# Optimization experiments

Measured on AMD Instinct MI355X. Metric: run time of the kernel, lower is better.

Reference implementation:

```python
import jax, jax.numpy as jnp
import numpy as np
from jax import lax

K = 3          # kernel size
PAD = 1        # (K-1)//2
C = 64         # channels
RED = 16       # channel-attention reduction


def conv2d(x, w, b=None):
    # x [B,C,H,W], w [O,I,kh,kw]
    out = lax.conv_general_dilated(x, w, (1, 1), 'SAME',
                                   dimension_numbers=('NCHW', 'OIHW', 'NCHW'))
    if b is not None:
        out = out + b[None, :, None, None]
    return out


def rcab(x, w1, b1, w2, b2, caw1, cab1, caw2, cab2):
    res = conv2d(x, w1, b1)
    res = jax.nn.relu(res)
    res = conv2d(res, w2, b2)
    # channel attention: global avg pool -> 1x1 conv -> relu -> 1x1 conv -> sigmoid
    y = jnp.mean(res, axis=(2, 3), keepdims=True)
    y = jax.nn.relu(conv2d(y, caw1, cab1))
    y = jax.nn.sigmoid(conv2d(y, caw2, cab2))
    return res * y + x


def deform_conv(x, inter, fea, off_w, off_b, mask_w, mask_b, weight):
    # Modulated deformable conv: offsets/mask predicted from concat(inter, fea).
    B, Cc, H, W = x.shape
    KK = K * K
    guide = jnp.concatenate([inter, fea], axis=1)
    offset = conv2d(guide, off_w, off_b)                    # [B, 2*KK, H, W]
    mask = 2.0 * jax.nn.sigmoid(conv2d(guide, mask_w, mask_b))  # [B, KK, H, W]
    off = offset.reshape(B, KK, 2, H, W)
    oy, ox = off[:, :, 0], off[:, :, 1]                     # [B, KK, H, W]

    ky = (jnp.arange(KK) // K - PAD).astype(x.dtype)        # kernel tap y offsets
    kx = (jnp.arange(KK) % K - PAD).astype(x.dtype)
    ii = jnp.arange(H, dtype=x.dtype)[None, None, :, None]
    jj = jnp.arange(W, dtype=x.dtype)[None, None, None, :]
    ys = ii + ky[None, :, None, None] + oy                  # [B, KK, H, W]
    xs = jj + kx[None, :, None, None] + ox

    y0 = jnp.floor(ys); x0 = jnp.floor(xs)
    wy1 = ys - y0; wy0 = 1.0 - wy1
    wx1 = xs - x0; wx0 = 1.0 - wx1
    y0i = y0.astype(jnp.int32); x0i = x0.astype(jnp.int32)
    y1i = y0i + 1; x1i = x0i + 1

    x_flat = x.reshape(B, Cc, H * W)

    def gather(yi, xi):
        valid = ((yi >= 0) & (yi < H) & (xi >= 0) & (xi < W)).astype(x.dtype)
        idx = jnp.clip(yi, 0, H - 1) * W + jnp.clip(xi, 0, W - 1)   # [B,KK,H,W]
        idx = idx.reshape(B, KK * H * W)
        g = jax.vmap(lambda f, i: jnp.take(f, i, axis=1))(x_flat, idx)
        return g.reshape(B, Cc, KK, H, W) * valid[:, None]

    val = (gather(y0i, x0i) * (wy0 * wx0)[:, None]
           + gather(y0i, x1i) * (wy0 * wx1)[:, None]
           + gather(y1i, x0i) * (wy1 * wx0)[:, None]
           + gather(y1i, x1i) * (wy1 * wx1)[:, None])     # [B,C,KK,H,W]
    val = val * mask[:, None]
    w_flat = weight.reshape(weight.shape[0], Cc, KK)        # [O,I,KK]
    return jnp.einsum('bckhw,ock->bohw', val, w_flat)


def setup_inputs() -> dict:
    key = jax.random.key(0)
    ks = jax.random.split(key, 20)
    B, H, W = 4, 192, 192
    f32 = jnp.float32
    d = {
        'x':     jax.random.normal(ks[0], (B, C, H, W), f32),
        'inter': jax.random.normal(ks[1], (B, C, H, W), f32),
        'fea':   jax.random.normal(ks[2], (B, C, H, W), f32),
        # RCAB
        'rcab_w1': jax.random.normal(ks[3], (C, C, 3, 3), f32) * 0.05,
        'rcab_b1': jnp.zeros((C,), f32),
        'rcab_w2': jax.random.normal(ks[4], (C, C, 3, 3), f32) * 0.05,
        'rcab_b2': jnp.zeros((C,), f32),
        'ca_w1': jax.random.normal(ks[5], (C // RED, C, 1, 1), f32) * 0.05,
        'ca_b1': jnp.zeros((C // RED,), f32),
        'ca_w2': jax.random.normal(ks[6], (C, C // RED, 1, 1), f32) * 0.05,
        'ca_b2': jnp.zeros((C,), f32),
        # deformable conv offset/mask branch (input = concat(inter, fea) -> 2C)
        'off_w': jax.random.normal(ks[7], (2 * K * K, 2 * C, 3, 3), f32) * 0.01,
        'off_b': jnp.zeros((2 * K * K,), f32),
        'mask_w': jax.random.normal(ks[8], (K * K, 2 * C, 3, 3), f32) * 0.01,
        'mask_b': jnp.zeros((K * K,), f32),
        'deform_w': jax.random.normal(ks[9], (C, C, K, K), f32) * 0.05,
        # final conv
        'conv_w': jax.random.normal(ks[10], (C, C, 3, 3), f32) * 0.05,
        'conv_b': jnp.zeros((C,), f32),
    }
    return d


def reference(x, inter, fea, rcab_w1, rcab_b1, rcab_w2, rcab_b2,
              ca_w1, ca_b1, ca_w2, ca_b2,
              off_w, off_b, mask_w, mask_b, deform_w, conv_w, conv_b):
    out1 = rcab(x, rcab_w1, rcab_b1, rcab_w2, rcab_b2, ca_w1, ca_b1, ca_w2, ca_b2)
    out2 = deform_conv(out1, inter, fea, off_w, off_b, mask_w, mask_b, deform_w)
    return conv2d(out2 + out1, conv_w, conv_b)
```

## Files before the change

kernel.cpp:

```cpp
#include <hip/hip_runtime.h>
#include <hip/hip_bf16.h>
#include <hip/hip_fp16.h>
#include <math.h>

#define HSZ 192
#define WSZ 192
#define HWSZ (192*192)
#define PH 194
#define PP (PH*PH)
#define NB 4

typedef __attribute__((ext_vector_type(8))) short short8;
typedef __attribute__((ext_vector_type(4))) float f32x4;

__device__ inline unsigned short f2bf(float f) { __hip_bfloat16 h = __float2bfloat16(f); return *(unsigned short*)&h; }
__device__ inline float bf2f(__hip_bfloat16 h) { return __bfloat162float(h); }
__device__ inline float bflo(unsigned u) { return __uint_as_float(u << 16); }
__device__ inline float bfhi(unsigned u) { return __uint_as_float(u & 0xffff0000u); }

#define GLDS(SRC, DST) __builtin_amdgcn_global_load_lds( \
    (const __attribute__((address_space(1))) unsigned int*)(const void*)(SRC), \
    (__attribute__((address_space(3))) unsigned int*)(void*)(DST), 16, 0, 0)

#define MFMA(A,B,C) __builtin_amdgcn_mfma_f32_16x16x32_bf16((A),(B),(C),0,0,0)

__global__ void zb2_k(__hip_bfloat16* xn, __hip_bfloat16* r1, __hip_bfloat16* out1,
                      __hip_bfloat16* cat) {
  int job = blockIdx.y;
  __hip_bfloat16* buf = job == 0 ? xn : job == 1 ? r1 : job == 2 ? out1 : cat;
  int Cn = (job == 3) ? 128 : 64;
  int cg8 = Cn >> 3;
  int tot = NB * 772 * cg8;
  int idx = blockIdx.x * 256 + threadIdx.x;
  if (idx >= tot) return;
  int cg = idx % cg8; int rem = idx / cg8;
  int e = rem % 772; int b = rem / 772;
  int h, w2;
  if (e < 194) { h = 0; w2 = e; }
  else if (e < 388) { h = 193; w2 = e - 194; }
  else if (e < 580) { h = e - 388 + 1; w2 = 0; }
  else { h = e - 580 + 1; w2 = 193; }
  uint4 z = make_uint4(0, 0, 0, 0);
  *(uint4*)&buf[(((size_t)b * PH + h) * PH + w2) * Cn + cg * 8] = z;
}

__global__ void wts_k(const float* __restrict__ rw1, const float* __restrict__ rw2,
                      const float* __restrict__ cw, const float* __restrict__ offw,
                      const float* __restrict__ maskw, const float* __restrict__ offb,
                      const float* __restrict__ maskb, const float* __restrict__ dwv,
                      short* wt1, short* wt2c, short* wtf, short* wtom, float* ob,
                      short* wtb, float* meanz) {
  int job = blockIdx.y;
  int idx = blockIdx.x * 256 + threadIdx.x;
  if (job < 3) {
    const float* src = job == 0 ? rw1 : job == 1 ? rw2 : cw;
    short* dst = job == 0 ? wt1 : job == 1 ? wt2c : wtf;
    int kk = idx >> 12, rem = idx & 4095;
    int co = rem >> 6, ci = rem & 63;
    dst[idx] = (short)f2bf(src[(co * 64 + ci) * 9 + kk]);
  } else if (job == 3) {
    int kk = idx >> 12, rem = idx & 4095;
    int co = rem >> 7, ci = rem & 127;
    float v = 0.f;
    if (co < 18) v = offw[(co * 128 + ci) * 9 + kk];
    else if (co < 27) v = maskw[((co - 18) * 128 + ci) * 9 + kk];
    wtom[idx] = (short)f2bf(v);
    if (idx < 32) ob[idx] = idx < 18 ? offb[idx] : (idx < 27 ? maskb[idx - 18] : 0.f);
  } else {
    int o = idx / 576, rem = idx - o * 576;
    int kk = rem >> 6, ci = rem & 63;
    wtb[idx] = (short)f2bf(dwv[(o * 64 + ci) * 9 + kk]);
    if (blockIdx.x == 0 && threadIdx.x < 256) meanz[threadIdx.x] = 0.f;
  }
}

__global__ __launch_bounds__(256) void cvt_k(const float* __restrict__ x,
    const float* __restrict__ inter, const float* __restrict__ fea,
    __hip_bfloat16* __restrict__ xn, __hip_bfloat16* __restrict__ cat) {
  int job = blockIdx.z;
  const float* src = job == 0 ? x : job == 1 ? inter : fea;
  __hip_bfloat16* dst = job == 0 ? xn : cat;
  int Cdst = job == 0 ? 64 : 128;
  int coff = job == 2 ? 64 : 0;
  __shared__ float s[64][65];
  int p0 = blockIdx.x * 64; int b = blockIdx.y;
  int lane = threadIdx.x & 63, g = threadIdx.x >> 6;
#pragma unroll
  for (int i = 0; i < 16; ++i) {
    int c = i * 4 + g;
    s[c][lane] = src[((size_t)b * 64 + c) * HWSZ + p0 + lane];
  }
  __syncthreads();
  int pix = threadIdx.x >> 2, cg = threadIdx.x & 3;
  int h = p0 / WSZ, w0 = p0 - h * WSZ + pix;
  size_t addr = (((size_t)b * PH + h + 1) * PH + 1 + w0) * Cdst + coff + cg * 16;
  unsigned pk2[8];
#pragma unroll
  for (int t = 0; t < 8; ++t)
    pk2[t] = (unsigned)f2bf(s[cg * 16 + 2 * t][pix]) | ((unsigned)f2bf(s[cg * 16 + 2 * t + 1][pix]) << 16);
  *(uint4*)&dst[addr]     = make_uint4(pk2[0], pk2[1], pk2[2], pk2[3]);
  *(uint4*)&dst[addr + 8] = make_uint4(pk2[4], pk2[5], pk2[6], pk2[7]);
}

template<int OUT_MODE, bool RELU, bool MEANACC>
__global__ __launch_bounds__(256, 3) void conv_mfma_k(
    const __hip_bfloat16* __restrict__ inp, const short* __restrict__ wt,
    const float* __restrict__ bias, __hip_bfloat16* __restrict__ outB,
    float* __restrict__ outF, float* __restrict__ meanout) {
  int flat = (blockIdx.x & 7) * 96 + (blockIdx.x >> 3);
  const int b = flat / 192, h = flat - (flat / 192) * 192;
  const int tid = threadIdx.x, lane = tid & 63, wid = tid >> 6;
  const int q = lane >> 4, r16 = lane & 15;
  __shared__ __align__(16) short tile[2][200 * 64];
  __shared__ float smean[4][64];

  const __hip_bfloat16* base = inp + ((size_t)b * PH + h) * (PH * 64);
#define STAGE(BUF, R) do { \
    const char* gb_ = (const char*)(base + (size_t)(R) * (PH * 64)); \
    for (int s_ = wid; s_ < 25; s_ += 4) { \
      int pix_ = 8 * s_ + (lane >> 3); \
      const char* src_ = gb_ + pix_ * 128 + ((((lane & 7) ^ ((lane >> 3) & 7))) << 4); \
      GLDS(src_, tile[BUF] + s_ * 512); \
    } \
  } while (0)

  STAGE(0, 0);

  f32x4 acc[3][4];
  if (OUT_MODE == 0) {
#pragma unroll
    for (int nf = 0; nf < 4; ++nf) {
      float4 bv = *(const float4*)&bias[nf * 16 + q * 4];
      f32x4 v; v[0] = bv.x; v[1] = bv.y; v[2] = bv.z; v[3] = bv.w;
      acc[0][nf] = v; acc[1][nf] = v; acc[2][nf] = v;
    }
  } else {
#pragma unroll
    for (int nf = 0; nf < 4; ++nf) {
      float bs = bias[nf * 16 + r16];
      f32x4 v; v[0] = bs; v[1] = bs; v[2] = bs; v[3] = bs;
      acc[0][nf] = v; acc[1][nf] = v; acc[2][nf] = v;
    }
  }

  short8 bfr[2][2][4];
  {
    const short* wk0 = wt + r16 * 64 + q * 8;
#pragma unroll
    for (int nf = 0; nf < 4; ++nf) {
      bfr[0][0][nf] = *(const short8*)(wk0 + nf * 1024);
      bfr[0][1][nf] = *(const short8*)(wk0 + nf * 1024 + 32);
    }
  }
  __syncthreads();

  const int wm0 = wid * 48;
#pragma unroll
  for (int ky = 0; ky < 3; ++ky) {
    const int cb = ky & 1;
    if (ky < 2) STAGE(cb ^ 1, ky + 1);
#pragma unroll
    for (int kx = 0; kx < 3; ++kx) {
      const int kk = ky * 3 + kx;
      const int cur = kk & 1;
      if (kk < 8) {
        const short* wk = wt + (kk + 1) * 4096 + r16 * 64 + q * 8;
#pragma unroll
        for (int nf = 0; nf < 4; ++nf) {
          bfr[cur ^ 1][0][nf] = *(const short8*)(wk + nf * 1024);
          bfr[cur ^ 1][1][nf] = *(const short8*)(wk + nf * 1024 + 32);
        }
      }
#pragma unroll
      for (int mf = 0; mf < 3; ++mf) {
        int pix = wm0 + mf * 16 + r16 + kx;
        const char* ab = (const char*)tile[cb] + pix * 128;
        int sw = (pix & 7) << 4;
        short8 a0 = *(const short8*)(ab + ((q << 4) ^ sw));
        short8 a1 = *(const short8*)(ab + (((q + 4) << 4) ^ sw));
#pragma unroll
        for (int nf = 0; nf < 4; ++nf) {
          if (OUT_MODE == 0) {
            acc[mf][nf] = MFMA(bfr[cur][0][nf], a0, acc[mf][nf]);
            acc[mf][nf] = MFMA(bfr[cur][1][nf], a1, acc[mf][nf]);
          } else {
            acc[mf][nf] = MFMA(a0, bfr[cur][0][nf], acc[mf][nf]);
            acc[mf][nf] = MFMA(a1, bfr[cur][1][nf], acc[mf][nf]);
          }
        }
      }
    }
    __syncthreads();
  }
#undef STAGE

  if (MEANACC) {
    float t[4][4];
#pragma unroll
    for (int nf = 0; nf < 4; ++nf)
#pragma unroll
      for (int rg = 0; rg < 4; ++rg)
        t[nf][rg] = acc[0][nf][rg] + acc[1][nf][rg] + acc[2][nf][rg];
#pragma unroll
    for (int m = 1; m < 16; m <<= 1)
#pragma unroll
      for (int nf = 0; nf < 4; ++nf)
#pragma unroll
        for (int rg = 0; rg < 4; ++rg)
          t[nf][rg] += __shfl_xor(t[nf][rg], m);
    if (r16 == 0)
#pragma unroll
      for (int nf = 0; nf < 4; ++nf)
#pragma unroll
        for (int rg = 0; rg < 4; ++rg)
          smean[wid][nf * 16 + q * 4 + rg] = t[nf][rg];
    __syncthreads();
    if (tid < 64)
      atomicAdd(&meanout[b * 64 + tid],
                (smean[0][tid] + smean[1][tid] + smean[2][tid] + smean[3][tid]) * (1.f / 36864.f));
  }

  if (OUT_MODE == 0) {
#pragma unroll
    for (int mf = 0; mf < 3; ++mf)
#pragma unroll
      for (int nf = 0; nf < 4; ++nf) {
        f32x4 v = acc[mf][nf];
        if (RELU) { v[0] = fmaxf(v[0], 0.f); v[1] = fmaxf(v[1], 0.f); v[2] = fmaxf(v[2], 0.f); v[3] = fmaxf(v[3], 0.f); }
        unsigned lo = (unsigned)f2bf(v[0]) | ((unsigned)f2bf(v[1]) << 16);
        unsigned hi = (unsigned)f2bf(v[2]) | ((unsigned)f2bf(v[3]) << 16);
        int pix = wm0 + mf * 16 + r16;
        int byteoff = (pix * 128 + nf * 32 + q * 8) ^ ((pix & 7) << 4);
        *(uint2*)((char*)tile[1] + byteoff) = make_uint2(lo, hi);
      }
    __syncthreads();
    char* orow = (char*)outB + ((((size_t)b * PH + h + 1) * PH + 1) * 64) * 2;
    for (int s = wid; s < 24; s += 4) {
      int pix = 8 * s + (lane >> 3);
      int g16 = ((lane & 7) ^ (pix & 7)) << 4;
      uint4 d = *(const uint4*)((const char*)tile[1] + pix * 128 + g16);
      *(uint4*)(orow + pix * 128 + ((lane & 7) << 4)) = d;
    }
  } else {
    float* ob2 = outF + (size_t)b * 64 * HWSZ + h * WSZ;
#pragma unroll
    for (int mf = 0; mf < 3; ++mf)
#pragma unroll
      for (int nf = 0; nf < 4; ++nf) {
        int pix0 = wm0 + mf * 16 + q * 4;
        int co = nf * 16 + r16;
        *(f32x4*)&ob2[(size_t)co * HWSZ + pix0] = acc[mf][nf];
      }
  }
}

__global__ __launch_bounds__(256, 3) void offmask_mfma_k(
    const __hip_bfloat16* __restrict__ cat, const short* __restrict__ wt2,
    const float* __restrict__ ob, float* __restrict__ om) {
  const int h = blockIdx.x, b = blockIdx.y;
  const int tid = threadIdx.x, lane = tid & 63, wid = tid >> 6;
  const int q = lane >> 4, r16 = lane & 15;
  __shared__ __align__(16) short tile[200 * 128];

  f32x4 acc[3][2];
#pragma unroll
  for (int nf = 0; nf < 2; ++nf) {
    float bs = ob[nf * 16 + r16];
    f32x4 v; v[0] = bs; v[1] = bs; v[2] = bs; v[3] = bs;
    acc[0][nf] = v; acc[1][nf] = v; acc[2][nf] = v;
  }
  const char* gb = (const char*)(cat + ((size_t)b * PH + h) * (PH * 128));
  const int wm0 = wid * 48;

  short8 bfr[2][4][2];
  {
    const short* wk0 = wt2 + r16 * 128 + q * 8;
#pragma unroll
    for (int c4 = 0; c4 < 4; ++c4) {
      bfr[0][c4][0] = *(const short8*)(wk0 + c4 * 32);
      bfr[0][c4][1] = *(const short8*)(wk0 + 2048 + c4 * 32);
    }
  }

#pragma unroll
  for (int r = 0; r < 3; ++r) {
    __syncthreads();
    for (int s = wid; s < 50; s += 4) {
      int pix = 4 * s + (lane >> 4);
      const char* src = gb + (size_t)r * (PH * 256) + pix * 256
                      + ((((lane & 15) ^ (pix & 15))) << 4);
      GLDS(src, tile + s * 512);
    }
    __syncthreads();
#pragma unroll
    for (int kx = 0; kx < 3; ++kx) {
      const int kk = r * 3 + kx;
      const int cur = kk & 1;
      if (kk < 8) {
        const short* wk = wt2 + (kk + 1) * 4096 + r16 * 128 + q * 8;
#pragma unroll
        for (int c4 = 0; c4 < 4; ++c4) {
          bfr[cur ^ 1][c4][0] = *(const short8*)(wk + c4 * 32);
          bfr[cur ^ 1][c4][1] = *(const short8*)(wk + 2048 + c4 * 32);
        }
      }
#pragma unroll
      for (int mf = 0; mf < 3; ++mf) {
        int pix = wm0 + mf * 16 + r16 + kx;
        const char* ab = (const char*)tile + pix * 256;
        int sw = (pix & 15) << 4;
        short8 a0 = *(const short8*)(ab + ((q << 4) ^ sw));
        short8 a1 = *(const short8*)(ab + (((4 + q) << 4) ^ sw));
        short8 a2 = *(const short8*)(ab + (((8 + q) << 4) ^ sw));
        short8 a3 = *(const short8*)(ab + (((12 + q) << 4) ^ sw));
        acc[mf][0] = MFMA(a0, bfr[cur][0][0], acc[mf][0]); acc[mf][1] = MFMA(a0, bfr[cur][0][1], acc[mf][1]);
        acc[mf][0] = MFMA(a1, bfr[cur][1][0], acc[mf][0]); acc[mf][1] = MFMA(a1, bfr[cur][1][1], acc[mf][1]);
        acc[mf][0] = MFMA(a2, bfr[cur][2][0], acc[mf][0]); acc[mf][1] = MFMA(a2, bfr[cur][2][1], acc[mf][1]);
        acc[mf][0] = MFMA(a3, bfr[cur][3][0], acc[mf][0]); acc[mf][1] = MFMA(a3, bfr[cur][3][1], acc[mf][1]);
      }
    }
  }
#pragma unroll
  for (int mf = 0; mf < 3; ++mf)
#pragma unroll
    for (int nf = 0; nf < 2; ++nf) {
      int co = nf * 16 + r16;
      if (co < 27) {
        f32x4 v = acc[mf][nf];
        if (co >= 18) {
          v[0] = 2.f / (1.f + expf(-v[0])); v[1] = 2.f / (1.f + expf(-v[1]));
          v[2] = 2.f / (1.f + expf(-v[2])); v[3] = 2.f / (1.f + expf(-v[3]));
        }
        *(f32x4*)&om[((size_t)(b * 27 + co)) * HWSZ + h * WSZ + wm0 + mf * 16 + q * 4] = v;
      }
    }
}

__global__ __launch_bounds__(256) void out1_k(const __hip_bfloat16* __restrict__ res, const __hip_bfloat16* __restrict__ xn,
    const float* __restrict__ mean, const float* __restrict__ w1, const float* __restrict__ b1,
    const float* __restrict__ w2, const float* __restrict__ b2,
    __hip_bfloat16* __restrict__ out1) {
  int idx = blockIdx.x * 256 + threadIdx.x;
  int b = idx / 294912; int rem = idx - b * 294912;
  int p = rem >> 3, c8 = rem & 7;
  int lane = threadIdx.x & 63, wid = threadIdx.x >> 6;

  __shared__ float s_t[4];
  {
    float prod = w1[wid * 64 + lane] * mean[b * 64 + lane];
#pragma unroll
    for (int m = 1; m < 64; m <<= 1) prod += __shfl_xor(prod, m);
    if (lane == 0) s_t[wid] = fmaxf(prod + b1[wid], 0.f);
  }
  __syncthreads();
  float t0 = s_t[0], t1 = s_t[1], t2 = s_t[2], t3 = s_t[3];

  int hh = p / WSZ, ww = p - hh * WSZ;
  size_t off = ((size_t)b * PP + (size_t)(hh + 1) * PH + ww + 1) * 64 + c8 * 8;
  const __hip_bfloat16* rp = res + off;
  const __hip_bfloat16* xp = xn + off;
  __hip_bfloat16* op = out1 + off;
  unsigned pk[4];
#pragma unroll
  for (int t = 0; t < 4; ++t) {
    float y0, y1;
    {
      int c = c8 * 8 + 2 * t;
      const float4 wv0 = *(const float4*)&w2[c * 4];
      const float4 wv1 = *(const float4*)&w2[(c + 1) * 4];
      float v0 = b2[c]     + wv0.x * t0 + wv0.y * t1 + wv0.z * t2 + wv0.w * t3;
      float v1 = b2[c + 1] + wv1.x * t0 + wv1.y * t1 + wv1.z * t2 + wv1.w * t3;
      y0 = 1.f / (1.f + expf(-v0));
      y1 = 1.f / (1.f + expf(-v1));
    }
    float o0 = bf2f(rp[2 * t]) * y0 + bf2f(xp[2 * t]);
    float o1 = bf2f(rp[2 * t + 1]) * y1 + bf2f(xp[2 * t + 1]);
    pk[t] = (unsigned)f2bf(o0) | ((unsigned)f2bf(o1) << 16);
  }
  *(uint4*)op = make_uint4(pk[0], pk[1], pk[2], pk[3]);
}

__global__ __launch_bounds__(256) void deform_mfma_k(
    const __hip_bfloat16* __restrict__ nhwc, const float* __restrict__ om,
    const short* __restrict__ wtb, __hip_bfloat16* __restrict__ fin) {
  int blk = (blockIdx.x & 7) * 288 + (blockIdx.x >> 3);
  int b = blk / 576;
  int p0 = (blk - b * 576) * 64;
  int tid = threadIdx.x, lane = tid & 63, wid = tid >> 6;
  int q = lane >> 4, r16 = lane & 15;
  __shared__ __align__(16) short sA[2][64][64];
  __shared__ __half2 s_bw[2][9][64];
  __shared__ int s_pk[9][64];

  const float* omb = om + (size_t)b * 27 * HWSZ + p0;
  for (int e = tid; e < 576; e += 256) {
    int kk = e >> 6, pix = e & 63;
    int p = p0 + pix;
    int h = p / WSZ, w2 = p - h * WSZ;
    float oy = omb[(size_t)(2 * kk) * HWSZ + pix];
    float ox = omb[(size_t)(2 * kk + 1) * HWSZ + pix];
    float m2 = omb[(size_t)(18 + kk) * HWSZ + pix];
    float ys = (float)(h + kk / 3 - 1) + oy;
    float xs = (float)(w2 + kk % 3 - 1) + ox;
    float y0f = floorf(ys), x0f = floorf(xs);
    float wy1 = ys - y0f, wx1 = xs - x0f;
    float wy0 = 1.f - wy1, wx0 = 1.f - wx1;
    int y0 = (int)y0f, x0i = (int)x0f;
    int y1 = y0 + 1, x1 = x0i + 1;
    float vy0 = (y0 >= 0 && y0 < HSZ) ? 1.f : 0.f;
    float vx0 = (x0i >= 0 && x0i < WSZ) ? 1.f : 0.f;
    float vy1 = (y1 >= 0 && y1 < HSZ) ? 1.f : 0.f;
    float vx1 = (x1 >= 0 && x1 < WSZ) ? 1.f : 0.f;
    int y0c = min(max(y0, 0), HSZ - 1), x0c = min(max(x0i, 0), WSZ - 1);
    int y1c = min(max(y1, 0), HSZ - 1), x1c = min(max(x1, 0), WSZ - 1);
    s_bw[0][kk][pix] = __floats2half2_rn(wy0 * wx0 * m2 * vy0 * vx0, wy0 * wx1 * m2 * vy0 * vx1);
    s_bw[1][kk][pix] = __floats2half2_rn(wy1 * wx0 * m2 * vy1 * vx0, wy1 * wx1 * m2 * vy1 * vx1);
    s_pk[kk][pix] = ((((y0c + 1) * PH) + x0c + 1) << 2) | ((y1c - y0c) << 1) | (x1c - x0c);
  }
  __syncthreads();

  const __hip_bfloat16* nb = nhwc + (size_t)b * PP * 64;
  const int spix = tid >> 2, lg = tid & 3;
  const int rsw = (r16 & 7) << 4;

  uint4 Pa0, Pb0, Qa0, Qb0, Ra0, Rb0, Sa0, Sb0;
  uint4 Pa1, Pb1, Qa1, Qb1, Ra1, Rb1, Sa1, Sb1;
  float2 wab0, wcd0, wab1, wcd1;

#define ISSUE_R(KK, Pa,Pb,Qa,Qb,Ra,Rb,Sa,Sb, Wab, Wcd) do { \
    Wab = __half22float2(s_bw[0][KK][spix]); \
    Wcd = __half22float2(s_bw[1][KK][spix]); \
    int pk_ = s_pk[KK][spix]; \
    int i00_ = pk_ >> 2, dy_ = (pk_ >> 1) & 1, dx_ = pk_ & 1; \
    const __hip_bfloat16* g_ = nb + (size_t)i00_ * 64 + lg * 16; \
    Pa = *(const uint4*)g_;                     Pb = *(const uint4*)(g_ + 8); \
    Qa = *(const uint4*)(g_ + dx_ * 64);        Qb = *(const uint4*)(g_ + dx_ * 64 + 8); \
    Ra = *(const uint4*)(g_ + dy_ * (PH * 64)); Rb = *(const uint4*)(g_ + dy_ * (PH * 64) + 8); \
    Sa = *(const uint4*)(g_ + (dy_ * PH + dx_) * 64); Sb = *(const uint4*)(g_ + (dy_ * PH + dx_) * 64 + 8); \
  } while (0)
#define CMB(J, PA,QA,RA,SA, Wab, Wcd, OUT) do { \
    const unsigned* pa_ = (const unsigned*)&PA; const unsigned* qa_ = (const unsigned*)&QA; \
    const unsigned* ra_ = (const unsigned*)&RA; const unsigned* sa_ = (const unsigned*)&SA; \
    float lo_ = Wab.x * bflo(pa_[J]) + Wab.y * bflo(qa_[J]) + Wcd.x * bflo(ra_[J]) + Wcd.y * bflo(sa_[J]); \
    float hi_ = Wab.x * bfhi(pa_[J]) + Wab.y * bfhi(qa_[J]) + Wcd.x * bfhi(ra_[J]) + Wcd.y * bfhi(sa_[J]); \
    OUT = (unsigned)f2bf(lo_) | ((unsigned)f2bf(hi_) << 16); \
  } while (0)
#define CSTORE_R(BUFOFF, Pa,Pb,Qa,Qb,Ra,Rb,Sa,Sb, Wab, Wcd) do { \
    unsigned oa_[4], ob_[4]; \
    CMB(0, Pa,Qa,Ra,Sa, Wab, Wcd, oa_[0]); CMB(1, Pa,Qa,Ra,Sa, Wab, Wcd, oa_[1]); \
    CMB(2, Pa,Qa,Ra,Sa, Wab, Wcd, oa_[2]); CMB(3, Pa,Qa,Ra,Sa, Wab, Wcd, oa_[3]); \
    CMB(0, Pb,Qb,Rb,Sb, Wab, Wcd, ob_[0]); CMB(1, Pb,Qb,Rb,Sb, Wab, Wcd, ob_[1]); \
    CMB(2, Pb,Qb,Rb,Sb, Wab, Wcd, ob_[2]); CMB(3, Pb,Qb,Rb,Sb, Wab, Wcd, ob_[3]); \
    char* dst_ = (char*)sA + (BUFOFF) + spix * 128; \
    *(uint4*)(dst_ + ((((lg * 2) ^ (spix & 7))) << 4))     = make_uint4(oa_[0], oa_[1], oa_[2], oa_[3]); \
    *(uint4*)(dst_ + ((((lg * 2 + 1) ^ (spix & 7))) << 4)) = make_uint4(ob_[0], ob_[1], ob_[2], ob_[3]); \
  } while (0)

  ISSUE_R(0, Pa0,Pb0,Qa0,Qb0,Ra0,Rb0,Sa0,Sb0, wab0, wcd0);
  CSTORE_R(0, Pa0,Pb0,Qa0,Qb0,Ra0,Rb0,Sa0,Sb0, wab0, wcd0);
  ISSUE_R(1, Pa0,Pb0,Qa0,Qb0,Ra0,Rb0,Sa0,Sb0, wab0, wcd0);
  ISSUE_R(2, Pa1,Pb1,Qa1,Qb1,Ra1,Rb1,Sa1,Sb1, wab1, wcd1);

  f32x4 acc0 = (f32x4){0.f, 0.f, 0.f, 0.f};
  f32x4 acc1 = (f32x4){0.f, 0.f, 0.f, 0.f};
  f32x4 acc2 = (f32x4){0.f, 0.f, 0.f, 0.f};
  f32x4 acc3 = (f32x4){0.f, 0.f, 0.f, 0.f};
  const short* wrow = wtb + (size_t)(wid * 16 + r16) * 576;
  const char* a0base = (const char*)sA + r16 * 128;
  const char* a1base = (const char*)sA + (r16 + 16) * 128;
  const char* a2base = (const char*)sA + (r16 + 32) * 128;
  const char* a3base = (const char*)sA + (r16 + 48) * 128;

#pragma unroll
  for (int kk = 0; kk < 9; ++kk) {
    const int bo = (kk & 1) * 8192;
    __syncthreads();
#pragma unroll
    for (int s = 0; s < 2; ++s) {
      short8 wf = *(const short8*)(wrow + kk * 64 + s * 32 + q * 8);
      int off = bo + ((s * 64 + q * 16) ^ rsw);
      acc0 = MFMA(wf, *(const short8*)(a0base + off), acc0);
      acc1 = MFMA(wf, *(const short8*)(a1base + off), acc1);
      acc2 = MFMA(wf, *(const short8*)(a2base + off), acc2);
      acc3 = MFMA(wf, *(const short8*)(a3base + off), acc3);
    }
    if (kk < 8) {
      const int nbo = ((kk + 1) & 1) * 8192;
      if ((kk & 1) == 0) {
        CSTORE_R(nbo, Pa0,Pb0,Qa0,Qb0,Ra0,Rb0,Sa0,Sb0, wab0, wcd0);
        if (kk + 3 <= 8) ISSUE_R(kk + 3, Pa0,Pb0,Qa0,Qb0,Ra0,Rb0,Sa0,Sb0, wab0, wcd0);
      } else {
        CSTORE_R(nbo, Pa1,Pb1,Qa1,Qb1,Ra1,Rb1,Sa1,Sb1, wab1, wcd1);
        if (kk + 3 <= 8) ISSUE_R(kk + 3, Pa1,Pb1,Qa1,Qb1,Ra1,Rb1,Sa1,Sb1, wab1, wcd1);
      }
    }
  }

  int h0 = p0 / WSZ, w0 = p0 - h0 * WSZ;
  size_t ro = ((size_t)(h0 + 1) * PH + w0 + 1) * 64;
  const __hip_bfloat16* resid = nb + ro;
  __hip_bfloat16* fp = fin + (size_t)b * PP * 64 + ro;
#pragma unroll
  for (int nf = 0; nf < 4; ++nf) {
    f32x4 av = nf == 0 ? acc0 : nf == 1 ? acc1 : nf == 2 ? acc2 : acc3;
    int pix = r16 + nf * 16;
    int co = wid * 16 + q * 4;
    const unsigned* rr = (const unsigned*)(resid + (size_t)pix * 64 + co);
    unsigned r0 = rr[0], r1 = rr[1];
    float o0 = av[0] + bflo(r0);
    float o1 = av[1] + bfhi(r0);
    float o2 = av[2] + bflo(r1);
    float o3 = av[3] + bfhi(r1);
    uint2 pk2 = make_uint2((unsigned)f2bf(o0) | ((unsigned)f2bf(o1) << 16),
                           (unsigned)f2bf(o2) | ((unsigned)f2bf(o3) << 16));
    *(uint2*)(fp + (size_t)pix * 64 + co) = pk2;
  }
#undef ISSUE_R
#undef CMB
#undef CSTORE_R
}

extern "C" void kernel_launch(void* const* d_in, const int* in_sizes, int n_in,
                              void* d_out, int out_size, void* d_ws, size_t ws_size,
                              hipStream_t stream) {
  (void)in_sizes; (void)n_in; (void)out_size; (void)ws_size;
  const float* x     = (const float*)d_in[0];
  const float* inter = (const float*)d_in[1];
  const float* fea   = (const float*)d_in[2];
  const float* rw1   = (const float*)d_in[3];
  const float* rb1   = (const float*)d_in[4];
  const float* rw2   = (const float*)d_in[5];
  const float* rb2   = (const float*)d_in[6];
  const float* caw1  = (const float*)d_in[7];
  const float* cab1  = (const float*)d_in[8];
  const float* caw2  = (const float*)d_in[9];
  const float* cab2  = (const float*)d_in[10];
  const float* offw  = (const float*)d_in[11];
  const float* offb  = (const float*)d_in[12];
  const float* maskw = (const float*)d_in[13];
  const float* maskb = (const float*)d_in[14];
  const float* dw    = (const float*)d_in[15];
  const float* cw    = (const float*)d_in[16];
  const float* cb    = (const float*)d_in[17];

  char* w = (char*)d_ws;
  const size_t P64 = (size_t)NB * PP * 64 * 2 + 4096;
  const size_t PCAT = (size_t)NB * PP * 128 * 2 + 4096;
  __hip_bfloat16* xn   = (__hip_bfloat16*)(w);
  __hip_bfloat16* r1   = (__hip_bfloat16*)(w + P64);
  __hip_bfloat16* res  = (__hip_bfloat16*)(w + 2 * P64);
  __hip_bfloat16* out1 = (__hip_bfloat16*)(w + 3 * P64);
  __hip_bfloat16* cat  = (__hip_bfloat16*)(w + 4 * P64);
  char* tail = w + 4 * P64 + PCAT;
  short* wt1  = (short*)tail; tail += 73728;
  short* wt2c = (short*)tail; tail += 73728;
  short* wtf  = (short*)tail; tail += 73728;
  short* wtom = (short*)tail; tail += 73728;
  float* obb  = (float*)tail; tail += 128;
  short* wtb  = (short*)tail; tail += 73728;
  float* mean = (float*)tail; tail += 1024;
  float* omb  = (float*)res;
  __hip_bfloat16* fin = r1;

  zb2_k<<<dim3(194, 4), 256, 0, stream>>>(xn, r1, out1, cat);
  wts_k<<<dim3(144, 5), 256, 0, stream>>>(rw1, rw2, cw, offw, maskw, offb, maskb, dw,
                                          wt1, wt2c, wtf, wtom, obb, wtb, mean);
  cvt_k<<<dim3(576, 4, 3), 256, 0, stream>>>(x, inter, fea, xn, cat);

  conv_mfma_k<0, true , false><<<768, 256, 0, stream>>>(xn, wt1, rb1, r1, nullptr, nullptr);
  conv_mfma_k<0, false, true ><<<768, 256, 0, stream>>>(r1, wt2c, rb2, res, nullptr, mean);
  out1_k<<<4608, 256, 0, stream>>>(res, xn, mean, caw1, cab1, caw2, cab2, out1);
  offmask_mfma_k<<<dim3(192, 4), 256, 0, stream>>>(cat, wtom, obb, omb);
  deform_mfma_k<<<NB * 576, 256, 0, stream>>>(out1, omb, wtb, fin);
  conv_mfma_k<1, false, false><<<768, 256, 0, stream>>>(fin, wtf, cb, nullptr, (float*)d_out, nullptr);
}
```

Baseline: 255.6 us.

## Merge conv1 and offset/mask conv into one launch, widen deform blocks

```diff
diff --git a/kernel.cpp b/kernel.cpp
--- a/kernel.cpp
+++ b/kernel.cpp
@@ -24,10 +24,10 @@
 
 #define MFMA(A,B,C) __builtin_amdgcn_mfma_f32_16x16x32_bf16((A),(B),(C),0,0,0)
 
-__global__ void zb2_k(__hip_bfloat16* xn, __hip_bfloat16* r1, __hip_bfloat16* out1,
+__global__ void zb2_k(__hip_bfloat16* xn, __hip_bfloat16* r1, __hip_bfloat16* res,
                       __hip_bfloat16* cat) {
   int job = blockIdx.y;
-  __hip_bfloat16* buf = job == 0 ? xn : job == 1 ? r1 : job == 2 ? out1 : cat;
+  __hip_bfloat16* buf = job == 0 ? xn : job == 1 ? r1 : job == 2 ? res : cat;
   int Cn = (job == 3) ? 128 : 64;
   int cg8 = Cn >> 3;
   int tot = NB * 772 * cg8;
@@ -103,16 +103,14 @@
 }
 
 template<int OUT_MODE, bool RELU, bool MEANACC>
-__global__ __launch_bounds__(256, 3) void conv_mfma_k(
+__device__ __forceinline__ void conv_body(int vbid, short* tbuf, float* smean,
     const __hip_bfloat16* __restrict__ inp, const short* __restrict__ wt,
     const float* __restrict__ bias, __hip_bfloat16* __restrict__ outB,
     float* __restrict__ outF, float* __restrict__ meanout) {
-  int flat = (blockIdx.x & 7) * 96 + (blockIdx.x >> 3);
+  int flat = (vbid & 7) * 96 + (vbid >> 3);
   const int b = flat / 192, h = flat - (flat / 192) * 192;
   const int tid = threadIdx.x, lane = tid & 63, wid = tid >> 6;
   const int q = lane >> 4, r16 = lane & 15;
-  __shared__ __align__(16) short tile[2][200 * 64];
-  __shared__ float smean[4][64];
 
   const __hip_bfloat16* base = inp + ((size_t)b * PH + h) * (PH * 64);
 #define STAGE(BUF, R) do { \
@@ -120,7 +118,7 @@
     for (int s_ = wid; s_ < 25; s_ += 4) { \
       int pix_ = 8 * s_ + (lane >> 3); \
       const char* src_ = gb_ + pix_ * 128 + ((((lane & 7) ^ ((lane >> 3) & 7))) << 4); \
-      GLDS(src_, tile[BUF] + s_ * 512); \
+      GLDS(src_, tbuf + (BUF) * 12800 + s_ * 512); \
     } \
   } while (0)
 
@@ -174,7 +172,7 @@
 #pragma unroll
       for (int mf = 0; mf < 3; ++mf) {
         int pix = wm0 + mf * 16 + r16 + kx;
-        const char* ab = (const char*)tile[cb] + pix * 128;
+        const char* ab = (const char*)(tbuf + cb * 12800) + pix * 128;
         int sw = (pix & 7) << 4;
         short8 a0 = *(const short8*)(ab + ((q << 4) ^ sw));
         short8 a1 = *(const short8*)(ab + (((q + 4) << 4) ^ sw));
@@ -213,14 +211,15 @@
       for (int nf = 0; nf < 4; ++nf)
 #pragma unroll
         for (int rg = 0; rg < 4; ++rg)
-          smean[wid][nf * 16 + q * 4 + rg] = t[nf][rg];
+          smean[wid * 64 + nf * 16 + q * 4 + rg] = t[nf][rg];
     __syncthreads();
     if (tid < 64)
       atomicAdd(&meanout[b * 64 + tid],
-                (smean[0][tid] + smean[1][tid] + smean[2][tid] + smean[3][tid]) * (1.f / 36864.f));
+                (smean[tid] + smean[64 + tid] + smean[128 + tid] + smean[192 + tid]) * (1.f / 36864.f));
   }
 
   if (OUT_MODE == 0) {
+    short* t1 = tbuf + 12800;
 #pragma unroll
     for (int mf = 0; mf < 3; ++mf)
 #pragma unroll
@@ -231,14 +230,14 @@
         unsigned hi = (unsigned)f2bf(v[2]) | ((unsigned)f2bf(v[3]) << 16);
         int pix = wm0 + mf * 16 + r16;
         int byteoff = (pix * 128 + nf * 32 + q * 8) ^ ((pix & 7) << 4);
-        *(uint2*)((char*)tile[1] + byteoff) = make_uint2(lo, hi);
+        *(uint2*)((char*)t1 + byteoff) = make_uint2(lo, hi);
       }
     __syncthreads();
     char* orow = (char*)outB + ((((size_t)b * PH + h + 1) * PH + 1) * 64) * 2;
     for (int s = wid; s < 24; s += 4) {
       int pix = 8 * s + (lane >> 3);
       int g16 = ((lane & 7) ^ (pix & 7)) << 4;
-      uint4 d = *(const uint4*)((const char*)tile[1] + pix * 128 + g16);
+      uint4 d = *(const uint4*)((const char*)t1 + pix * 128 + g16);
       *(uint4*)(orow + pix * 128 + ((lane & 7) << 4)) = d;
     }
   } else {
@@ -254,13 +253,13 @@
   }
 }
 
-__global__ __launch_bounds__(256, 3) void offmask_mfma_k(
+__device__ __forceinline__ void offmask_body(int vbid, short* tbuf,
     const __hip_bfloat16* __restrict__ cat, const short* __restrict__ wt2,
     const float* __restrict__ ob, float* __restrict__ om) {
-  const int h = blockIdx.x, b = blockIdx.y;
+  int flat = (vbid & 7) * 96 + (vbid >> 3);
+  const int b = flat / 192, h = flat - (flat / 192) * 192;
   const int tid = threadIdx.x, lane = tid & 63, wid = tid >> 6;
   const int q = lane >> 4, r16 = lane & 15;
-  __shared__ __align__(16) short tile[200 * 128];
 
   f32x4 acc[3][2];
 #pragma unroll
@@ -289,7 +288,7 @@
       int pix = 4 * s + (lane >> 4);
       const char* src = gb + (size_t)r * (PH * 256) + pix * 256
                       + ((((lane & 15) ^ (pix & 15))) << 4);
-      GLDS(src, tile + s * 512);
+      GLDS(src, tbuf + s * 512);
     }
     __syncthreads();
 #pragma unroll
@@ -307,7 +306,7 @@
 #pragma unroll
       for (int mf = 0; mf < 3; ++mf) {
         int pix = wm0 + mf * 16 + r16 + kx;
-        const char* ab = (const char*)tile + pix * 256;
+        const char* ab = (const char*)tbuf + pix * 256;
         int sw = (pix & 15) << 4;
         short8 a0 = *(const short8*)(ab + ((q << 4) ^ sw));
         short8 a1 = *(const short8*)(ab + (((4 + q) << 4) ^ sw));
@@ -336,10 +335,33 @@
     }
 }
 
-__global__ __launch_bounds__(256) void out1_k(const __hip_bfloat16* __restrict__ res, const __hip_bfloat16* __restrict__ xn,
+template<int OUT_MODE, bool RELU, bool MEANACC>
+__global__ __launch_bounds__(256, 3) void conv_mfma_k(
+    const __hip_bfloat16* __restrict__ inp, const short* __restrict__ wt,
+    const float* __restrict__ bias, __hip_bfloat16* __restrict__ outB,
+    float* __restrict__ outF, float* __restrict__ meanout) {
+  __shared__ __align__(16) short tile[2 * 12800];
+  __shared__ float smean[256];
+  conv_body<OUT_MODE, RELU, MEANACC>(blockIdx.x, tile, smean, inp, wt, bias, outB, outF, meanout);
+}
+
+__global__ __launch_bounds__(256, 3) void c1om_k(
+    const __hip_bfloat16* __restrict__ xn, const short* __restrict__ wt1,
+    const float* __restrict__ rb1, __hip_bfloat16* __restrict__ r1,
+    const __hip_bfloat16* __restrict__ cat, const short* __restrict__ wtom,
+    const float* __restrict__ obb, float* __restrict__ omb) {
+  __shared__ __align__(16) short tile[2 * 12800];
+  int g = blockIdx.x >> 3;
+  int vid = ((g >> 1) << 3) | (blockIdx.x & 7);
+  if ((g & 1) == 0)
+    conv_body<0, true, false>(vid, tile, nullptr, xn, wt1, rb1, r1, nullptr, nullptr);
+  else
+    offmask_body(vid, tile, cat, wtom, obb, omb);
+}
+
+__global__ __launch_bounds__(256) void out1_k(__hip_bfloat16* __restrict__ res, const __hip_bfloat16* __restrict__ xn,
     const float* __restrict__ mean, const float* __restrict__ w1, const float* __restrict__ b1,
-    const float* __restrict__ w2, const float* __restrict__ b2,
-    __hip_bfloat16* __restrict__ out1) {
+    const float* __restrict__ w2, const float* __restrict__ b2) {
   int idx = blockIdx.x * 256 + threadIdx.x;
   int b = idx / 294912; int rem = idx - b * 294912;
   int p = rem >> 3, c8 = rem & 7;
@@ -357,9 +379,8 @@
 
   int hh = p / WSZ, ww = p - hh * WSZ;
   size_t off = ((size_t)b * PP + (size_t)(hh + 1) * PH + ww + 1) * 64 + c8 * 8;
-  const __hip_bfloat16* rp = res + off;
+  __hip_bfloat16* rp = res + off;
   const __hip_bfloat16* xp = xn + off;
-  __hip_bfloat16* op = out1 + off;
   unsigned pk[4];
 #pragma unroll
   for (int t = 0; t < 4; ++t) {
@@ -377,24 +398,24 @@
     float o1 = bf2f(rp[2 * t + 1]) * y1 + bf2f(xp[2 * t + 1]);
     pk[t] = (unsigned)f2bf(o0) | ((unsigned)f2bf(o1) << 16);
   }
-  *(uint4*)op = make_uint4(pk[0], pk[1], pk[2], pk[3]);
-}
-
-__global__ __launch_bounds__(256) void deform_mfma_k(
+  *(uint4*)rp = make_uint4(pk[0], pk[1], pk[2], pk[3]);
+}
+
+__global__ __launch_bounds__(512) void deform_mfma_k(
     const __hip_bfloat16* __restrict__ nhwc, const float* __restrict__ om,
     const short* __restrict__ wtb, __hip_bfloat16* __restrict__ fin) {
-  int blk = (blockIdx.x & 7) * 288 + (blockIdx.x >> 3);
-  int b = blk / 576;
-  int p0 = (blk - b * 576) * 64;
+  int blk = (blockIdx.x & 7) * 144 + (blockIdx.x >> 3);
+  int b = blk / 288;
+  int p0 = (blk - b * 288) * 128;
   int tid = threadIdx.x, lane = tid & 63, wid = tid >> 6;
   int q = lane >> 4, r16 = lane & 15;
-  __shared__ __align__(16) short sA[2][64][64];
-  __shared__ __half2 s_bw[2][9][64];
-  __shared__ int s_pk[9][64];
+  __shared__ __align__(16) short sA[2][128][64];
+  __shared__ __half2 s_bw[2][9][128];
+  __shared__ int s_pk[9][128];
 
   const float* omb = om + (size_t)b * 27 * HWSZ + p0;
-  for (int e = tid; e < 576; e += 256) {
-    int kk = e >> 6, pix = e & 63;
+  for (int e = tid; e < 1152; e += 512) {
+    int kk = e >> 7, pix = e & 127;
     int p = p0 + pix;
     int h = p / WSZ, w2 = p - h * WSZ;
     float oy = omb[(size_t)(2 * kk) * HWSZ + pix];
@@ -465,15 +486,16 @@
   f32x4 acc1 = (f32x4){0.f, 0.f, 0.f, 0.f};
   f32x4 acc2 = (f32x4){0.f, 0.f, 0.f, 0.f};
   f32x4 acc3 = (f32x4){0.f, 0.f, 0.f, 0.f};
-  const short* wrow = wtb + (size_t)(wid * 16 + r16) * 576;
-  const char* a0base = (const char*)sA + r16 * 128;
-  const char* a1base = (const char*)sA + (r16 + 16) * 128;
-  const char* a2base = (const char*)sA + (r16 + 32) * 128;
-  const char* a3base = (const char*)sA + (r16 + 48) * 128;
+  const int cs = wid & 3, ph = wid >> 2;
+  const short* wrow = wtb + (size_t)(cs * 16 + r16) * 576;
+  const char* a0base = (const char*)sA + (ph * 64 + r16) * 128;
+  const char* a1base = (const char*)sA + (ph * 64 + r16 + 16) * 128;
+  const char* a2base = (const char*)sA + (ph * 64 + r16 + 32) * 128;
+  const char* a3base = (const char*)sA + (ph * 64 + r16 + 48) * 128;
 
 #pragma unroll
   for (int kk = 0; kk < 9; ++kk) {
-    const int bo = (kk & 1) * 8192;
+    const int bo = (kk & 1) * 16384;
     __syncthreads();
 #pragma unroll
     for (int s = 0; s < 2; ++s) {
@@ -485,7 +507,7 @@
       acc3 = MFMA(wf, *(const short8*)(a3base + off), acc3);
     }
     if (kk < 8) {
-      const int nbo = ((kk + 1) & 1) * 8192;
+      const int nbo = ((kk + 1) & 1) * 16384;
       if ((kk & 1) == 0) {
         CSTORE_R(nbo, Pa0,Pb0,Qa0,Qb0,Ra0,Rb0,Sa0,Sb0, wab0, wcd0);
         if (kk + 3 <= 8) ISSUE_R(kk + 3, Pa0,Pb0,Qa0,Qb0,Ra0,Rb0,Sa0,Sb0, wab0, wcd0);
@@ -496,16 +518,16 @@
     }
   }
 
-  int h0 = p0 / WSZ, w0 = p0 - h0 * WSZ;
-  size_t ro = ((size_t)(h0 + 1) * PH + w0 + 1) * 64;
-  const __hip_bfloat16* resid = nb + ro;
-  __hip_bfloat16* fp = fin + (size_t)b * PP * 64 + ro;
+  __hip_bfloat16* fb = fin + (size_t)b * PP * 64;
 #pragma unroll
   for (int nf = 0; nf < 4; ++nf) {
     f32x4 av = nf == 0 ? acc0 : nf == 1 ? acc1 : nf == 2 ? acc2 : acc3;
-    int pix = r16 + nf * 16;
-    int co = wid * 16 + q * 4;
-    const unsigned* rr = (const unsigned*)(resid + (size_t)pix * 64 + co);
+    int pix = ph * 64 + nf * 16 + r16;
+    int p = p0 + pix;
+    int hh = p / WSZ, ww = p - hh * WSZ;
+    size_t po = ((size_t)(hh + 1) * PH + ww + 1) * 64;
+    int co = cs * 16 + q * 4;
+    const unsigned* rr = (const unsigned*)(nb + po + co);
     unsigned r0 = rr[0], r1 = rr[1];
     float o0 = av[0] + bflo(r0);
     float o1 = av[1] + bfhi(r0);
@@ -513,7 +535,7 @@
     float o3 = av[3] + bfhi(r1);
     uint2 pk2 = make_uint2((unsigned)f2bf(o0) | ((unsigned)f2bf(o1) << 16),
                            (unsigned)f2bf(o2) | ((unsigned)f2bf(o3) << 16));
-    *(uint2*)(fp + (size_t)pix * 64 + co) = pk2;
+    *(uint2*)(fb + po + co) = pk2;
   }
 #undef ISSUE_R
 #undef CMB
@@ -549,7 +571,7 @@
   __hip_bfloat16* xn   = (__hip_bfloat16*)(w);
   __hip_bfloat16* r1   = (__hip_bfloat16*)(w + P64);
   __hip_bfloat16* res  = (__hip_bfloat16*)(w + 2 * P64);
-  __hip_bfloat16* out1 = (__hip_bfloat16*)(w + 3 * P64);
+  float* omb           = (float*)(w + 3 * P64);
   __hip_bfloat16* cat  = (__hip_bfloat16*)(w + 4 * P64);
   char* tail = w + 4 * P64 + PCAT;
   short* wt1  = (short*)tail; tail += 73728;
@@ -559,18 +581,16 @@
   float* obb  = (float*)tail; tail += 128;
   short* wtb  = (short*)tail; tail += 73728;
   float* mean = (float*)tail; tail += 1024;
-  float* omb  = (float*)res;
   __hip_bfloat16* fin = r1;
 
-  zb2_k<<<dim3(194, 4), 256, 0, stream>>>(xn, r1, out1, cat);
+  zb2_k<<<dim3(194, 4), 256, 0, stream>>>(xn, r1, res, cat);
   wts_k<<<dim3(144, 5), 256, 0, stream>>>(rw1, rw2, cw, offw, maskw, offb, maskb, dw,
                                           wt1, wt2c, wtf, wtom, obb, wtb, mean);
   cvt_k<<<dim3(576, 4, 3), 256, 0, stream>>>(x, inter, fea, xn, cat);
 
-  conv_mfma_k<0, true , false><<<768, 256, 0, stream>>>(xn, wt1, rb1, r1, nullptr, nullptr);
+  c1om_k<<<1536, 256, 0, stream>>>(xn, wt1, rb1, r1, cat, wtom, obb, omb);
   conv_mfma_k<0, false, true ><<<768, 256, 0, stream>>>(r1, wt2c, rb2, res, nullptr, mean);
-  out1_k<<<4608, 256, 0, stream>>>(res, xn, mean, caw1, cab1, caw2, cab2, out1);
-  offmask_mfma_k<<<dim3(192, 4), 256, 0, stream>>>(cat, wtom, obb, omb);
-  deform_mfma_k<<<NB * 576, 256, 0, stream>>>(out1, omb, wtb, fin);
+  out1_k<<<4608, 256, 0, stream>>>(res, xn, mean, caw1, cab1, caw2, cab2);
+  deform_mfma_k<<<NB * 288, 512, 0, stream>>>(res, omb, wtb, fin);
   conv_mfma_k<1, false, false><<<768, 256, 0, stream>>>(fin, wtf, cb, nullptr, (float*)d_out, nullptr);
 }
```

Result: slower. 342.0 us (+33.8%).

## Split conv output channels across 8 waves and run out1 update in place

Applied to the files above, without the earlier changes.

```diff
diff --git a/kernel.cpp b/kernel.cpp
--- a/kernel.cpp
+++ b/kernel.cpp
@@ -24,10 +24,10 @@
 
 #define MFMA(A,B,C) __builtin_amdgcn_mfma_f32_16x16x32_bf16((A),(B),(C),0,0,0)
 
-__global__ void zb2_k(__hip_bfloat16* xn, __hip_bfloat16* r1, __hip_bfloat16* out1,
+__global__ void zb2_k(__hip_bfloat16* xn, __hip_bfloat16* r1, __hip_bfloat16* res,
                       __hip_bfloat16* cat) {
   int job = blockIdx.y;
-  __hip_bfloat16* buf = job == 0 ? xn : job == 1 ? r1 : job == 2 ? out1 : cat;
+  __hip_bfloat16* buf = job == 0 ? xn : job == 1 ? r1 : job == 2 ? res : cat;
   int Cn = (job == 3) ? 128 : 64;
   int cg8 = Cn >> 3;
   int tot = NB * 772 * cg8;
@@ -103,58 +103,59 @@
 }
 
 template<int OUT_MODE, bool RELU, bool MEANACC>
-__global__ __launch_bounds__(256, 3) void conv_mfma_k(
+__global__ __launch_bounds__(512, 3) void conv_mfma_k(
     const __hip_bfloat16* __restrict__ inp, const short* __restrict__ wt,
     const float* __restrict__ bias, __hip_bfloat16* __restrict__ outB,
     float* __restrict__ outF, float* __restrict__ meanout) {
-  int flat = (blockIdx.x & 7) * 96 + (blockIdx.x >> 3);
+  __shared__ __align__(16) short tbuf[2 * 12800];
+  __shared__ float smean[256];
+  int flat = ((int)blockIdx.x & 7) * 96 + ((int)blockIdx.x >> 3);
   const int b = flat / 192, h = flat - (flat / 192) * 192;
   const int tid = threadIdx.x, lane = tid & 63, wid = tid >> 6;
   const int q = lane >> 4, r16 = lane & 15;
-  __shared__ __align__(16) short tile[2][200 * 64];
-  __shared__ float smean[4][64];
+  const int cw = wid >> 2;
+  const int wm0 = (wid & 3) * 48;
 
   const __hip_bfloat16* base = inp + ((size_t)b * PH + h) * (PH * 64);
 #define STAGE(BUF, R) do { \
     const char* gb_ = (const char*)(base + (size_t)(R) * (PH * 64)); \
-    for (int s_ = wid; s_ < 25; s_ += 4) { \
+    for (int s_ = wid; s_ < 25; s_ += 8) { \
       int pix_ = 8 * s_ + (lane >> 3); \
       const char* src_ = gb_ + pix_ * 128 + ((((lane & 7) ^ ((lane >> 3) & 7))) << 4); \
-      GLDS(src_, tile[BUF] + s_ * 512); \
+      GLDS(src_, tbuf + (BUF) * 12800 + s_ * 512); \
     } \
   } while (0)
 
   STAGE(0, 0);
 
-  f32x4 acc[3][4];
+  f32x4 acc[3][2];
   if (OUT_MODE == 0) {
 #pragma unroll
-    for (int nf = 0; nf < 4; ++nf) {
-      float4 bv = *(const float4*)&bias[nf * 16 + q * 4];
+    for (int nf = 0; nf < 2; ++nf) {
+      float4 bv = *(const float4*)&bias[(cw * 2 + nf) * 16 + q * 4];
       f32x4 v; v[0] = bv.x; v[1] = bv.y; v[2] = bv.z; v[3] = bv.w;
       acc[0][nf] = v; acc[1][nf] = v; acc[2][nf] = v;
     }
   } else {
 #pragma unroll
-    for (int nf = 0; nf < 4; ++nf) {
-      float bs = bias[nf * 16 + r16];
+    for (int nf = 0; nf < 2; ++nf) {
+      float bs = bias[(cw * 2 + nf) * 16 + r16];
       f32x4 v; v[0] = bs; v[1] = bs; v[2] = bs; v[3] = bs;
       acc[0][nf] = v; acc[1][nf] = v; acc[2][nf] = v;
     }
   }
 
-  short8 bfr[2][2][4];
+  short8 bfr[2][2][2];
   {
     const short* wk0 = wt + r16 * 64 + q * 8;
 #pragma unroll
-    for (int nf = 0; nf < 4; ++nf) {
-      bfr[0][0][nf] = *(const short8*)(wk0 + nf * 1024);
-      bfr[0][1][nf] = *(const short8*)(wk0 + nf * 1024 + 32);
+    for (int nf = 0; nf < 2; ++nf) {
+      bfr[0][0][nf] = *(const short8*)(wk0 + (cw * 2 + nf) * 1024);
+      bfr[0][1][nf] = *(const short8*)(wk0 + (cw * 2 + nf) * 1024 + 32);
     }
   }
   __syncthreads();
 
-  const int wm0 = wid * 48;
 #pragma unroll
   for (int ky = 0; ky < 3; ++ky) {
     const int cb = ky & 1;
@@ -166,20 +167,20 @@
       if (kk < 8) {
         const short* wk = wt + (kk + 1) * 4096 + r16 * 64 + q * 8;
 #pragma unroll
-        for (int nf = 0; nf < 4; ++nf) {
-          bfr[cur ^ 1][0][nf] = *(const short8*)(wk + nf * 1024);
-          bfr[cur ^ 1][1][nf] = *(const short8*)(wk + nf * 1024 + 32);
+        for (int nf = 0; nf < 2; ++nf) {
+          bfr[cur ^ 1][0][nf] = *(const short8*)(wk + (cw * 2 + nf) * 1024);
+          bfr[cur ^ 1][1][nf] = *(const short8*)(wk + (cw * 2 + nf) * 1024 + 32);
         }
       }
 #pragma unroll
       for (int mf = 0; mf < 3; ++mf) {
         int pix = wm0 + mf * 16 + r16 + kx;
-        const char* ab = (const char*)tile[cb] + pix * 128;
+        const char* ab = (const char*)(tbuf + cb * 12800) + pix * 128;
         int sw = (pix & 7) << 4;
         short8 a0 = *(const short8*)(ab + ((q << 4) ^ sw));
         short8 a1 = *(const short8*)(ab + (((q + 4) << 4) ^ sw));
 #pragma unroll
-        for (int nf = 0; nf < 4; ++nf) {
+        for (int nf = 0; nf < 2; ++nf) {
           if (OUT_MODE == 0) {
             acc[mf][nf] = MFMA(bfr[cur][0][nf], a0, acc[mf][nf]);
             acc[mf][nf] = MFMA(bfr[cur][1][nf], a1, acc[mf][nf]);
@@ -195,50 +196,54 @@
 #undef STAGE
 
   if (MEANACC) {
-    float t[4][4];
-#pragma unroll
-    for (int nf = 0; nf < 4; ++nf)
+    float t[2][4];
+#pragma unroll
+    for (int nf = 0; nf < 2; ++nf)
 #pragma unroll
       for (int rg = 0; rg < 4; ++rg)
         t[nf][rg] = acc[0][nf][rg] + acc[1][nf][rg] + acc[2][nf][rg];
 #pragma unroll
     for (int m = 1; m < 16; m <<= 1)
 #pragma unroll
-      for (int nf = 0; nf < 4; ++nf)
+      for (int nf = 0; nf < 2; ++nf)
 #pragma unroll
         for (int rg = 0; rg < 4; ++rg)
           t[nf][rg] += __shfl_xor(t[nf][rg], m);
     if (r16 == 0)
 #pragma unroll
-      for (int nf = 0; nf < 4; ++nf)
+      for (int nf = 0; nf < 2; ++nf)
 #pragma unroll
         for (int rg = 0; rg < 4; ++rg)
-          smean[wid][nf * 16 + q * 4 + rg] = t[nf][rg];
+          smean[wid * 32 + nf * 16 + q * 4 + rg] = t[nf][rg];
     __syncthreads();
-    if (tid < 64)
+    if (tid < 64) {
+      int half = tid >> 5, cl = tid & 31;
       atomicAdd(&meanout[b * 64 + tid],
-                (smean[0][tid] + smean[1][tid] + smean[2][tid] + smean[3][tid]) * (1.f / 36864.f));
+                (smean[(half * 4 + 0) * 32 + cl] + smean[(half * 4 + 1) * 32 + cl] +
+                 smean[(half * 4 + 2) * 32 + cl] + smean[(half * 4 + 3) * 32 + cl]) * (1.f / 36864.f));
+    }
   }
 
   if (OUT_MODE == 0) {
+    short* t1 = tbuf + 12800;
 #pragma unroll
     for (int mf = 0; mf < 3; ++mf)
 #pragma unroll
-      for (int nf = 0; nf < 4; ++nf) {
+      for (int nf = 0; nf < 2; ++nf) {
         f32x4 v = acc[mf][nf];
         if (RELU) { v[0] = fmaxf(v[0], 0.f); v[1] = fmaxf(v[1], 0.f); v[2] = fmaxf(v[2], 0.f); v[3] = fmaxf(v[3], 0.f); }
         unsigned lo = (unsigned)f2bf(v[0]) | ((unsigned)f2bf(v[1]) << 16);
         unsigned hi = (unsigned)f2bf(v[2]) | ((unsigned)f2bf(v[3]) << 16);
         int pix = wm0 + mf * 16 + r16;
-        int byteoff = (pix * 128 + nf * 32 + q * 8) ^ ((pix & 7) << 4);
-        *(uint2*)((char*)tile[1] + byteoff) = make_uint2(lo, hi);
+        int byteoff = (pix * 128 + (cw * 2 + nf) * 32 + q * 8) ^ ((pix & 7) << 4);
+        *(uint2*)((char*)t1 + byteoff) = make_uint2(lo, hi);
       }
     __syncthreads();
     char* orow = (char*)outB + ((((size_t)b * PH + h + 1) * PH + 1) * 64) * 2;
-    for (int s = wid; s < 24; s += 4) {
+    for (int s = wid; s < 24; s += 8) {
       int pix = 8 * s + (lane >> 3);
       int g16 = ((lane & 7) ^ (pix & 7)) << 4;
-      uint4 d = *(const uint4*)((const char*)tile[1] + pix * 128 + g16);
+      uint4 d = *(const uint4*)((const char*)t1 + pix * 128 + g16);
       *(uint4*)(orow + pix * 128 + ((lane & 7) << 4)) = d;
     }
   } else {
@@ -246,9 +251,9 @@
 #pragma unroll
     for (int mf = 0; mf < 3; ++mf)
 #pragma unroll
-      for (int nf = 0; nf < 4; ++nf) {
+      for (int nf = 0; nf < 2; ++nf) {
         int pix0 = wm0 + mf * 16 + q * 4;
-        int co = nf * 16 + r16;
+        int co = (cw * 2 + nf) * 16 + r16;
         *(f32x4*)&ob2[(size_t)co * HWSZ + pix0] = acc[mf][nf];
       }
   }
@@ -257,7 +262,8 @@
 __global__ __launch_bounds__(256, 3) void offmask_mfma_k(
     const __hip_bfloat16* __restrict__ cat, const short* __restrict__ wt2,
     const float* __restrict__ ob, float* __restrict__ om) {
-  const int h = blockIdx.x, b = blockIdx.y;
+  int flat = ((int)blockIdx.x & 7) * 96 + ((int)blockIdx.x >> 3);
+  const int b = flat / 192, h = flat - (flat / 192) * 192;
   const int tid = threadIdx.x, lane = tid & 63, wid = tid >> 6;
   const int q = lane >> 4, r16 = lane & 15;
   __shared__ __align__(16) short tile[200 * 128];
@@ -336,10 +342,9 @@
     }
 }
 
-__global__ __launch_bounds__(256) void out1_k(const __hip_bfloat16* __restrict__ res, const __hip_bfloat16* __restrict__ xn,
+__global__ __launch_bounds__(256) void out1_k(__hip_bfloat16* __restrict__ res, const __hip_bfloat16* __restrict__ xn,
     const float* __restrict__ mean, const float* __restrict__ w1, const float* __restrict__ b1,
-    const float* __restrict__ w2, const float* __restrict__ b2,
-    __hip_bfloat16* __restrict__ out1) {
+    const float* __restrict__ w2, const float* __restrict__ b2) {
   int idx = blockIdx.x * 256 + threadIdx.x;
   int b = idx / 294912; int rem = idx - b * 294912;
   int p = rem >> 3, c8 = rem & 7;
@@ -357,9 +362,8 @@
 
   int hh = p / WSZ, ww = p - hh * WSZ;
   size_t off = ((size_t)b * PP + (size_t)(hh + 1) * PH + ww + 1) * 64 + c8 * 8;
-  const __hip_bfloat16* rp = res + off;
+  __hip_bfloat16* rp = res + off;
   const __hip_bfloat16* xp = xn + off;
-  __hip_bfloat16* op = out1 + off;
   unsigned pk[4];
 #pragma unroll
   for (int t = 0; t < 4; ++t) {
@@ -377,13 +381,13 @@
     float o1 = bf2f(rp[2 * t + 1]) * y1 + bf2f(xp[2 * t + 1]);
     pk[t] = (unsigned)f2bf(o0) | ((unsigned)f2bf(o1) << 16);
   }
-  *(uint4*)op = make_uint4(pk[0], pk[1], pk[2], pk[3]);
+  *(uint4*)rp = make_uint4(pk[0], pk[1], pk[2], pk[3]);
 }
 
 __global__ __launch_bounds__(256) void deform_mfma_k(
     const __hip_bfloat16* __restrict__ nhwc, const float* __restrict__ om,
     const short* __restrict__ wtb, __hip_bfloat16* __restrict__ fin) {
-  int blk = (blockIdx.x & 7) * 288 + (blockIdx.x >> 3);
+  int blk = ((int)blockIdx.x & 7) * 288 + ((int)blockIdx.x >> 3);
   int b = blk / 576;
   int p0 = (blk - b * 576) * 64;
   int tid = threadIdx.x, lane = tid & 63, wid = tid >> 6;
@@ -549,7 +553,7 @@
   __hip_bfloat16* xn   = (__hip_bfloat16*)(w);
   __hip_bfloat16* r1   = (__hip_bfloat16*)(w + P64);
   __hip_bfloat16* res  = (__hip_bfloat16*)(w + 2 * P64);
-  __hip_bfloat16* out1 = (__hip_bfloat16*)(w + 3 * P64);
+  float* omb           = (float*)(w + 3 * P64);
   __hip_bfloat16* cat  = (__hip_bfloat16*)(w + 4 * P64);
   char* tail = w + 4 * P64 + PCAT;
   short* wt1  = (short*)tail; tail += 73728;
@@ -559,18 +563,17 @@
   float* obb  = (float*)tail; tail += 128;
   short* wtb  = (short*)tail; tail += 73728;
   float* mean = (float*)tail; tail += 1024;
-  float* omb  = (float*)res;
   __hip_bfloat16* fin = r1;
 
-  zb2_k<<<dim3(194, 4), 256, 0, stream>>>(xn, r1, out1, cat);
+  zb2_k<<<dim3(194, 4), 256, 0, stream>>>(xn, r1, res, cat);
   wts_k<<<dim3(144, 5), 256, 0, stream>>>(rw1, rw2, cw, offw, maskw, offb, maskb, dw,
                                           wt1, wt2c, wtf, wtom, obb, wtb, mean);
   cvt_k<<<dim3(576, 4, 3), 256, 0, stream>>>(x, inter, fea, xn, cat);
 
-  conv_mfma_k<0, true , false><<<768, 256, 0, stream>>>(xn, wt1, rb1, r1, nullptr, nullptr);
-  conv_mfma_k<0, false, true ><<<768, 256, 0, stream>>>(r1, wt2c, rb2, res, nullptr, mean);
-  out1_k<<<4608, 256, 0, stream>>>(res, xn, mean, caw1, cab1, caw2, cab2, out1);
-  offmask_mfma_k<<<dim3(192, 4), 256, 0, stream>>>(cat, wtom, obb, omb);
-  deform_mfma_k<<<NB * 576, 256, 0, stream>>>(out1, omb, wtb, fin);
-  conv_mfma_k<1, false, false><<<768, 256, 0, stream>>>(fin, wtf, cb, nullptr, (float*)d_out, nullptr);
-}
+  conv_mfma_k<0, true , false><<<768, 512, 0, stream>>>(xn, wt1, rb1, r1, nullptr, nullptr);
+  conv_mfma_k<0, false, true ><<<768, 512, 0, stream>>>(r1, wt2c, rb2, res, nullptr, mean);
+  out1_k<<<4608, 256, 0, stream>>>(res, xn, mean, caw1, cab1, caw2, cab2);
+  offmask_mfma_k<<<768, 256, 0, stream>>>(cat, wtom, obb, omb);
+  deform_mfma_k<<<NB * 576, 256, 0, stream>>>(res, omb, wtb, fin);
+  conv_mfma_k<1, false, false><<<768, 512, 0, stream>>>(fin, wtf, cb, nullptr, (float*)d_out, nullptr);
+}
```

Result: faster. 247.8 us (-3.1%).
